# Performance work log

Hardware: AMD Instinct MI355X
Metric: run time of the kernel (lower is better)

Reference implementation:

```python
import jax, jax.numpy as jnp
import numpy as np

NEG_SLOPE = 0.2


def add_self_loops(edge_index, num_nodes):
    loop = jnp.arange(num_nodes, dtype=edge_index.dtype)
    src = jnp.concatenate([edge_index[0], loop])
    dst = jnp.concatenate([edge_index[1], loop])
    return src, dst


def gat_conv(x, src, dst, W, att_src, att_dst, bias, heads, out_ch, concat):
    N = x.shape[0]
    h = (x @ W).reshape(N, heads, out_ch)                      # [N,H,C]
    a_src = jnp.sum(h * att_src, axis=-1)                      # [N,H]
    a_dst = jnp.sum(h * att_dst, axis=-1)                      # [N,H]
    e = a_src[src] + a_dst[dst]                                # [E,H]
    e = jax.nn.leaky_relu(e, NEG_SLOPE)
    # segment softmax over incoming edges of each destination node
    m = jax.ops.segment_max(e, dst, num_segments=N)            # [N,H]
    m = jnp.where(jnp.isfinite(m), m, 0.0)
    ex = jnp.exp(e - m[dst])
    s = jax.ops.segment_sum(ex, dst, num_segments=N)           # [N,H]
    alpha = ex / jnp.where(s[dst] > 0, s[dst], 1.0)            # [E,H]
    msg = alpha[:, :, None] * h[src]                           # [E,H,C]
    out = jax.ops.segment_sum(msg, dst, num_segments=N)        # [N,H,C]
    if concat:
        out = out.reshape(N, heads * out_ch)
    else:
        out = out.mean(axis=1)
    return out + bias


def setup_inputs() -> dict:
    key = jax.random.key(0)
    ks = jax.random.split(key, 10)
    N, F, E, H, C1 = 50000, 128, 800000, 8, 8
    x = jax.random.normal(ks[0], (N, F), dtype=jnp.float32)
    edge_index = jax.random.randint(ks[1], (2, E), 0, N, dtype=jnp.int64)
    sc = 0.1
    W1 = jax.random.normal(ks[2], (F, H * C1), dtype=jnp.float32) * sc
    a_src1 = jax.random.normal(ks[3], (H, C1), dtype=jnp.float32) * sc
    a_dst1 = jax.random.normal(ks[4], (H, C1), dtype=jnp.float32) * sc
    b1 = jnp.zeros((H * C1,), dtype=jnp.float32)
    W2 = jax.random.normal(ks[5], (H * C1, F), dtype=jnp.float32) * sc
    a_src2 = jax.random.normal(ks[6], (1, F), dtype=jnp.float32) * sc
    a_dst2 = jax.random.normal(ks[7], (1, F), dtype=jnp.float32) * sc
    b2 = jnp.zeros((F,), dtype=jnp.float32)
    return {"x": x, "edge_index": edge_index, "W1": W1, "a_src1": a_src1,
            "a_dst1": a_dst1, "b1": b1, "W2": W2, "a_src2": a_src2,
            "a_dst2": a_dst2, "b2": b2}


def reference(x, edge_index, W1, a_src1, a_dst1, b1, W2, a_src2, a_dst2, b2):
    N = x.shape[0]
    src, dst = add_self_loops(edge_index, N)
    h = gat_conv(x, src, dst, W1, a_src1, a_dst1, b1, heads=8, out_ch=8, concat=True)
    h = jax.nn.elu(h)
    out = gat_conv(h, src, dst, W2, a_src2, a_dst2, b2, heads=1, out_ch=x.shape[1], concat=True)
    return out
```

## Files before the change

kernel.cpp:

```cpp
#include <hip/hip_runtime.h>
#include <hip/hip_fp16.h>
#include <math.h>

#define NEG_SLOPE 0.2f

typedef _Float16 f16x8 __attribute__((ext_vector_type(8)));
typedef float    f32x4 __attribute__((ext_vector_type(4)));

__device__ __forceinline__ void get_edge(const int* __restrict__ ei, int E, int e,
                                         int& s, int& d) {
    if (e < E) { s = ei[e]; d = ei[E + e]; }
    else       { s = e - E; d = e - E; }
}

__global__ __launch_bounds__(256) void bucket_count(const int* __restrict__ ei, int E, int ET,
                                                    int* __restrict__ bcnt) {
    __shared__ int lhist[256];
    int t = threadIdx.x;
    lhist[t] = 0;
    __syncthreads();
    int start = blockIdx.x * 4096;
#pragma unroll
    for (int k = 0; k < 16; ++k) {
        int e = start + t + k * 256;
        if (e < ET) { int s, d; get_edge(ei, E, e, s, d); atomicAdd(&lhist[d >> 8], 1); }
    }
    __syncthreads();
    if (lhist[t] > 0) atomicAdd(&bcnt[t], lhist[t]);
}

__global__ void bucket_scan(const int* __restrict__ bcnt, int* __restrict__ bbase,
                            int* __restrict__ bcur, int* __restrict__ row_ptr,
                            int nbuck, int N, int ET) {
    __shared__ int buf[256];
    int t = threadIdx.x;
    int v = (t < nbuck) ? bcnt[t] : 0;
    buf[t] = v;
    __syncthreads();
    for (int off = 1; off < 256; off <<= 1) {
        int u = (t >= off) ? buf[t - off] : 0;
        __syncthreads();
        buf[t] += u;
        __syncthreads();
    }
    if (t < nbuck) { int ex = buf[t] - v; bbase[t] = ex; bcur[t] = ex; }
    if (t == 0) row_ptr[N] = ET;
}

__global__ __launch_bounds__(256) void bucket_scatter(const int* __restrict__ ei, int E, int ET,
                                                      int* __restrict__ bcur,
                                                      unsigned int* __restrict__ bstore,
                                                      int nbuck) {
    __shared__ int lhist[256], lbase[256], lrank[256], gbase[256];
    __shared__ unsigned int sbuf[4096];
    __shared__ int saddr[4096];
    int t = threadIdx.x;
    int start = blockIdx.x * 4096;
    int cnt = ET - start; if (cnt > 4096) cnt = 4096;
    lhist[t] = 0; lrank[t] = 0;
    __syncthreads();
    int mybuck[16]; unsigned int myval[16];
#pragma unroll
    for (int k = 0; k < 16; ++k) {
        int e = start + t + k * 256;
        mybuck[k] = -1;
        if (e < ET) {
            int s, d; get_edge(ei, E, e, s, d);
            mybuck[k] = d >> 8;
            myval[k] = ((unsigned int)d << 16) | (unsigned int)s;
            atomicAdd(&lhist[mybuck[k]], 1);
        }
    }
    __syncthreads();
    int v = lhist[t];
    lbase[t] = v;
    __syncthreads();
    for (int off = 1; off < 256; off <<= 1) {
        int u = (t >= off) ? lbase[t - off] : 0;
        __syncthreads();
        lbase[t] += u;
        __syncthreads();
    }
    int excl = lbase[t] - v;
    if (t < nbuck && v > 0) gbase[t] = atomicAdd(&bcur[t], v);
    __syncthreads();
    lbase[t] = excl;
    __syncthreads();
#pragma unroll
    for (int k = 0; k < 16; ++k) {
        int b = mybuck[k];
        if (b >= 0) {
            int r = atomicAdd(&lrank[b], 1);
            int idx = lbase[b] + r;
            sbuf[idx] = myval[k];
            saddr[idx] = gbase[b] + r;
        }
    }
    __syncthreads();
    for (int j = t; j < cnt; j += 256)
        bstore[saddr[j]] = sbuf[j];
}

__global__ __launch_bounds__(256) void bucket_csr(const unsigned int* __restrict__ bstore,
                                                  const int* __restrict__ bcnt,
                                                  const int* __restrict__ bbase,
                                                  int* __restrict__ row_ptr,
                                                  int* __restrict__ col, int N) {
    __shared__ int lcnt[256], lexcl[256], lrank[256];
    int b = blockIdx.x, t = threadIdx.x;
    int nb = bcnt[b], base = bbase[b];
    lcnt[t] = 0; lrank[t] = 0;
    __syncthreads();
    for (int i = t; i < nb; i += 256)
        atomicAdd(&lcnt[(bstore[base + i] >> 16) & 255], 1);
    __syncthreads();
    int v = lcnt[t];
    lexcl[t] = v;
    __syncthreads();
    for (int off = 1; off < 256; off <<= 1) {
        int u = (t >= off) ? lexcl[t - off] : 0;
        __syncthreads();
        lexcl[t] += u;
        __syncthreads();
    }
    int ex = lexcl[t] - v;
    __syncthreads();
    lexcl[t] = ex;
    __syncthreads();
    int node = (b << 8) + t;
    if (node < N) row_ptr[node] = base + ex;
    for (int i = t; i < nb; i += 256) {
        unsigned int pk = bstore[base + i];
        int d8 = (pk >> 16) & 255;
        int r = atomicAdd(&lrank[d8], 1);
        col[base + lexcl[d8] + r] = (int)(pk & 0xFFFFu);
    }
}

__global__ __launch_bounds__(256) void gemm1_kernel(const float* __restrict__ x,
                                                    const float* __restrict__ W,
                                                    const float* __restrict__ asrc,
                                                    const float* __restrict__ adst,
                                                    _Float16* __restrict__ hout,
                                                    float* __restrict__ av,
                                                    float* __restrict__ bv, int N,
                                                    int gblocks,
                                                    const float* __restrict__ W2,
                                                    const float* __restrict__ as2,
                                                    const float* __restrict__ ad2,
                                                    float* __restrict__ wa,
                                                    float* __restrict__ wb,
                                                    int* __restrict__ bcnt) {
    if (blockIdx.x == (unsigned)gblocks) {
        int k = threadIdx.x;
        bcnt[k] = 0;
        if (k < 64) {
            const float* wr = W2 + k * 128;
            float sa = 0.f, sb = 0.f;
#pragma unroll 8
            for (int c = 0; c < 128; ++c) {
                float w = wr[c];
                sa = fmaf(w, as2[c], sa);
                sb = fmaf(w, ad2[c], sb);
            }
            wa[k] = sa; wb[k] = sb;
        }
        return;
    }
    __shared__ unsigned int sWu[4096];
    for (int p = threadIdx.x; p < 4096; p += 256) {
        int frag = p >> 8;
        int lane = (p >> 2) & 63;
        int j2   = p & 3;
        int chunk = frag >> 2, nt = frag & 3;
        int k = chunk * 32 + ((lane >> 4) << 3) + (j2 << 1);
        int n = nt * 16 + (lane & 15);
        union { _Float16 h[2]; unsigned int u; } pk;
        pk.h[0] = (_Float16)W[k * 64 + n];
        pk.h[1] = (_Float16)W[(k + 1) * 64 + n];
        sWu[p] = pk.u;
    }
    __syncthreads();

    int lane = threadIdx.x & 63;
    int wid  = threadIdx.x >> 6;
    int rbase = blockIdx.x * 64 + wid * 16;
    int l15 = lane & 15, quad = lane >> 4;
    int rA = rbase + l15; if (rA >= N) rA = N - 1;

    const unsigned int* fragbase = &sWu[lane * 4];
    f32x4 z = {0.f, 0.f, 0.f, 0.f};
    f32x4 acc[4] = {z, z, z, z};

#pragma unroll
    for (int chunk = 0; chunk < 4; ++chunk) {
        const float* xp = x + (size_t)rA * 128 + chunk * 32 + quad * 8;
        float4 f0 = *((const float4*)xp);
        float4 f1 = *((const float4*)(xp + 4));
        f16x8 af;
        af[0] = (_Float16)f0.x; af[1] = (_Float16)f0.y;
        af[2] = (_Float16)f0.z; af[3] = (_Float16)f0.w;
        af[4] = (_Float16)f1.x; af[5] = (_Float16)f1.y;
        af[6] = (_Float16)f1.z; af[7] = (_Float16)f1.w;
#pragma unroll
        for (int t = 0; t < 4; ++t) {
            f16x8 bf = *((const f16x8*)(fragbase + (chunk * 4 + t) * 256));
            acc[t] = __builtin_amdgcn_mfma_f32_16x16x32_f16(af, bf, acc[t], 0, 0, 0);
        }
    }

    float asc[4], adc[4];
#pragma unroll
    for (int t = 0; t < 4; ++t) { asc[t] = asrc[t * 16 + l15]; adc[t] = adst[t * 16 + l15]; }
#pragma unroll
    for (int reg = 0; reg < 4; ++reg) {
        int r = rbase + quad * 4 + reg;
        bool ok = (r < N);
#pragma unroll
        for (int t = 0; t < 4; ++t) {
            float v = acc[t][reg];
            if (ok) hout[(size_t)r * 64 + t * 16 + l15] = (_Float16)v;
            float pa = v * asc[t], pb = v * adc[t];
            pa += __shfl_xor(pa, 1); pb += __shfl_xor(pb, 1);
            pa += __shfl_xor(pa, 2); pb += __shfl_xor(pb, 2);
            pa += __shfl_xor(pa, 4); pb += __shfl_xor(pb, 4);
            if (ok && (lane & 7) == 0) {
                int head = t * 2 + (l15 >> 3);
                av[r * 8 + head] = pa;
                bv[r * 8 + head] = pb;
            }
        }
    }
}

__global__ __launch_bounds__(512) void agg1_kernel(const int* __restrict__ rp,
                                                   const int* __restrict__ col,
                                                   const float* __restrict__ av,
                                                   const float* __restrict__ bv,
                                                   const __half* __restrict__ h1,
                                                   const float* __restrict__ b1,
                                                   const float* __restrict__ wa,
                                                   const float* __restrict__ wb,
                                                   _Float16* __restrict__ out1,
                                                   float* __restrict__ av2,
                                                   float* __restrict__ bv2, int N) {
    int node = blockIdx.x * 8 + (threadIdx.x >> 6);
    int lane = threadIdx.x & 63;
    if (node >= N) return;
    int g = lane >> 3, gl = lane & 7;
    int beg = rp[node], end = rp[node + 1];
    int last = end - 1;
    float bd = bv[node * 8 + gl];
    const uint4* hrow = (const uint4*)h1;

    uint4 z4 = {0u, 0u, 0u, 0u};
    int e = beg + g;
    int c0 = col[e      <= last ? e      : last];
    int c1 = col[e + 8  <= last ? e + 8  : last];
    int c2 = col[e + 16 <= last ? e + 16 : last];
    float av0 = 0.f, av1v = 0.f; uint4 h0 = z4, h1v = z4;
    if (e < end)     { av0  = av[c0 * 8 + gl]; h0  = hrow[(size_t)c0 * 8 + gl]; }
    if (e + 8 < end) { av1v = av[c1 * 8 + gl]; h1v = hrow[(size_t)c1 * 8 + gl]; }

    float s = 0.f, a0 = 0.f, a1 = 0.f, a2 = 0.f, a3 = 0.f,
          a4 = 0.f, a5 = 0.f, a6 = 0.f, a7 = 0.f;
    for (; e < end; e += 8) {
        float av2v = 0.f; uint4 h2 = z4;
        if (e + 16 < end) { av2v = av[c2 * 8 + gl]; h2 = hrow[(size_t)c2 * 8 + gl]; }
        int c3 = col[e + 24 <= last ? e + 24 : last];
        float l = av0 + bd;
        l = l > 0.f ? l : NEG_SLOPE * l;
        float w = __expf(l);
        float2 f0 = __half22float2(*(const __half2*)&h0.x);
        float2 f1 = __half22float2(*(const __half2*)&h0.y);
        float2 f2 = __half22float2(*(const __half2*)&h0.z);
        float2 f3 = __half22float2(*(const __half2*)&h0.w);
        s += w;
        a0 = fmaf(w, f0.x, a0); a1 = fmaf(w, f0.y, a1);
        a2 = fmaf(w, f1.x, a2); a3 = fmaf(w, f1.y, a3);
        a4 = fmaf(w, f2.x, a4); a5 = fmaf(w, f2.y, a5);
        a6 = fmaf(w, f3.x, a6); a7 = fmaf(w, f3.y, a7);
        av0 = av1v; h0 = h1v; av1v = av2v; h1v = h2; c2 = c3;
    }
#pragma unroll
    for (int off = 8; off < 64; off <<= 1) {
        s  += __shfl_xor(s, off);
        a0 += __shfl_xor(a0, off); a1 += __shfl_xor(a1, off);
        a2 += __shfl_xor(a2, off); a3 += __shfl_xor(a3, off);
        a4 += __shfl_xor(a4, off); a5 += __shfl_xor(a5, off);
        a6 += __shfl_xor(a6, off); a7 += __shfl_xor(a7, off);
    }
    float inv = 1.0f / s;
    float4 bb0 = ((const float4*)b1)[gl * 2];
    float4 bb1 = ((const float4*)b1)[gl * 2 + 1];
    float v0 = a0 * inv + bb0.x, v1 = a1 * inv + bb0.y;
    float v2 = a2 * inv + bb0.z, v3 = a3 * inv + bb0.w;
    float v4 = a4 * inv + bb1.x, v5 = a5 * inv + bb1.y;
    float v6 = a6 * inv + bb1.z, v7 = a7 * inv + bb1.w;
    v0 = v0 > 0.f ? v0 : expm1f(v0); v1 = v1 > 0.f ? v1 : expm1f(v1);
    v2 = v2 > 0.f ? v2 : expm1f(v2); v3 = v3 > 0.f ? v3 : expm1f(v3);
    v4 = v4 > 0.f ? v4 : expm1f(v4); v5 = v5 > 0.f ? v5 : expm1f(v5);
    v6 = v6 > 0.f ? v6 : expm1f(v6); v7 = v7 > 0.f ? v7 : expm1f(v7);
    float4 wa0 = ((const float4*)wa)[gl * 2], wa1 = ((const float4*)wa)[gl * 2 + 1];
    float4 wb0 = ((const float4*)wb)[gl * 2], wb1 = ((const float4*)wb)[gl * 2 + 1];
    float pa = v0 * wa0.x + v1 * wa0.y + v2 * wa0.z + v3 * wa0.w
             + v4 * wa1.x + v5 * wa1.y + v6 * wa1.z + v7 * wa1.w;
    float pb = v0 * wb0.x + v1 * wb0.y + v2 * wb0.z + v3 * wb0.w
             + v4 * wb1.x + v5 * wb1.y + v6 * wb1.z + v7 * wb1.w;
    pa += __shfl_xor(pa, 1); pb += __shfl_xor(pb, 1);
    pa += __shfl_xor(pa, 2); pb += __shfl_xor(pb, 2);
    pa += __shfl_xor(pa, 4); pb += __shfl_xor(pb, 4);
    if (lane == 0) { av2[node] = pa; bv2[node] = pb; }
    if (g == 0) {
        f16x8 o;
        o[0] = (_Float16)v0; o[1] = (_Float16)v1; o[2] = (_Float16)v2; o[3] = (_Float16)v3;
        o[4] = (_Float16)v4; o[5] = (_Float16)v5; o[6] = (_Float16)v6; o[7] = (_Float16)v7;
        ((f16x8*)out1)[(size_t)node * 8 + gl] = o;
    }
}

__global__ __launch_bounds__(512) void agg2_kernel(const int* __restrict__ rp,
                                                   const int* __restrict__ col,
                                                   const float* __restrict__ av,
                                                   const float* __restrict__ bv,
                                                   const __half* __restrict__ out1,
                                                   float* __restrict__ agg64, int N) {
    int node = blockIdx.x * 8 + (threadIdx.x >> 6);
    int lane = threadIdx.x & 63;
    if (node >= N) return;
    int g = lane >> 3, gl = lane & 7;
    int beg = rp[node], end = rp[node + 1];
    int last = end - 1;
    float bd = bv[node];
    const uint4* hrow = (const uint4*)out1;

    uint4 z4 = {0u, 0u, 0u, 0u};
    int e = beg + g;
    int c0 = col[e      <= last ? e      : last];
    int c1 = col[e + 8  <= last ? e + 8  : last];
    int c2 = col[e + 16 <= last ? e + 16 : last];
    float av0 = 0.f, av1v = 0.f; uint4 h0 = z4, h1v = z4;
    if (e < end)     { av0  = av[c0]; h0  = hrow[(size_t)c0 * 8 + gl]; }
    if (e + 8 < end) { av1v = av[c1]; h1v = hrow[(size_t)c1 * 8 + gl]; }

    float s = 0.f, a0 = 0.f, a1 = 0.f, a2 = 0.f, a3 = 0.f,
          a4 = 0.f, a5 = 0.f, a6 = 0.f, a7 = 0.f;
    for (; e < end; e += 8) {
        float av2v = 0.f; uint4 h2 = z4;
        if (e + 16 < end) { av2v = av[c2]; h2 = hrow[(size_t)c2 * 8 + gl]; }
        int c3 = col[e + 24 <= last ? e + 24 : last];
        float l = av0 + bd;
        l = l > 0.f ? l : NEG_SLOPE * l;
        float w = __expf(l);
        float2 f0 = __half22float2(*(const __half2*)&h0.x);
        float2 f1 = __half22float2(*(const __half2*)&h0.y);
        float2 f2 = __half22float2(*(const __half2*)&h0.z);
        float2 f3 = __half22float2(*(const __half2*)&h0.w);
        s += w;
        a0 = fmaf(w, f0.x, a0); a1 = fmaf(w, f0.y, a1);
        a2 = fmaf(w, f1.x, a2); a3 = fmaf(w, f1.y, a3);
        a4 = fmaf(w, f2.x, a4); a5 = fmaf(w, f2.y, a5);
        a6 = fmaf(w, f3.x, a6); a7 = fmaf(w, f3.y, a7);
        av0 = av1v; h0 = h1v; av1v = av2v; h1v = h2; c2 = c3;
    }
#pragma unroll
    for (int off = 8; off < 64; off <<= 1) {
        s  += __shfl_xor(s, off);
        a0 += __shfl_xor(a0, off); a1 += __shfl_xor(a1, off);
        a2 += __shfl_xor(a2, off); a3 += __shfl_xor(a3, off);
        a4 += __shfl_xor(a4, off); a5 += __shfl_xor(a5, off);
        a6 += __shfl_xor(a6, off); a7 += __shfl_xor(a7, off);
    }
    if (g == 0) {
        float inv = 1.0f / s;
        ((float4*)agg64)[(size_t)node * 16 + gl * 2] =
            make_float4(a0 * inv, a1 * inv, a2 * inv, a3 * inv);
        ((float4*)agg64)[(size_t)node * 16 + gl * 2 + 1] =
            make_float4(a4 * inv, a5 * inv, a6 * inv, a7 * inv);
    }
}

__global__ __launch_bounds__(256) void gemm2_kernel(const float* __restrict__ he,
                                                    const float* __restrict__ W,
                                                    const float* __restrict__ b2,
                                                    float* __restrict__ dout, int N) {
    __shared__ unsigned int sWu[4096];
    for (int p = threadIdx.x; p < 4096; p += 256) {
        int frag = p >> 8;
        int lane = (p >> 2) & 63;
        int j2   = p & 3;
        int chunk = frag >> 3, nt = frag & 7;
        int k = chunk * 32 + ((lane >> 4) << 3) + (j2 << 1);
        int n = nt * 16 + (lane & 15);
        union { _Float16 h[2]; unsigned int u; } pk;
        pk.h[0] = (_Float16)W[k * 128 + n];
        pk.h[1] = (_Float16)W[(k + 1) * 128 + n];
        sWu[p] = pk.u;
    }
    __syncthreads();

    int lane = threadIdx.x & 63;
    int wid  = threadIdx.x >> 6;
    int rbase = blockIdx.x * 64 + wid * 16;
    int l15 = lane & 15, quad = lane >> 4;
    int rA = rbase + l15; if (rA >= N) rA = N - 1;

    const unsigned int* fragbase = &sWu[lane * 4];
    f32x4 z = {0.f, 0.f, 0.f, 0.f};
    f32x4 acc[8] = {z, z, z, z, z, z, z, z};

#pragma unroll
    for (int chunk = 0; chunk < 2; ++chunk) {
        const float* xp = he + (size_t)rA * 64 + chunk * 32 + quad * 8;
        float4 f0 = *((const float4*)xp);
        float4 f1 = *((const float4*)(xp + 4));
        f16x8 af;
        af[0] = (_Float16)f0.x; af[1] = (_Float16)f0.y;
        af[2] = (_Float16)f0.z; af[3] = (_Float16)f0.w;
        af[4] = (_Float16)f1.x; af[5] = (_Float16)f1.y;
        af[6] = (_Float16)f1.z; af[7] = (_Float16)f1.w;
#pragma unroll
        for (int t = 0; t < 8; ++t) {
            f16x8 bf = *((const f16x8*)(fragbase + (chunk * 8 + t) * 256));
            acc[t] = __builtin_amdgcn_mfma_f32_16x16x32_f16(af, bf, acc[t], 0, 0, 0);
        }
    }

    float bcol[8];
#pragma unroll
    for (int t = 0; t < 8; ++t) bcol[t] = b2[t * 16 + l15];
#pragma unroll
    for (int reg = 0; reg < 4; ++reg) {
        int r = rbase + quad * 4 + reg;
        if (r < N) {
#pragma unroll
            for (int t = 0; t < 8; ++t)
                dout[(size_t)r * 128 + t * 16 + l15] = acc[t][reg] + bcol[t];
        }
    }
}

extern "C" void kernel_launch(void* const* d_in, const int* in_sizes, int n_in,
                              void* d_out, int out_size, void* d_ws, size_t ws_size,
                              hipStream_t stream) {
    const float* x      = (const float*)d_in[0];
    const int*   ei     = (const int*)  d_in[1];
    const float* W1     = (const float*)d_in[2];
    const float* a_src1 = (const float*)d_in[3];
    const float* a_dst1 = (const float*)d_in[4];
    const float* b1     = (const float*)d_in[5];
    const float* W2     = (const float*)d_in[6];
    const float* a_src2 = (const float*)d_in[7];
    const float* a_dst2 = (const float*)d_in[8];
    const float* b2     = (const float*)d_in[9];
    float* dout = (float*)d_out;

    const int N  = in_sizes[0] / 128;
    const int E  = in_sizes[1] / 2;
    const int ET = E + N;
    const int NBUCK = (N + 255) >> 8;
    const int NBLKA = (ET + 4095) >> 12;

    char* wsb = (char*)d_ws;
    _Float16* h1   = (_Float16*)wsb; wsb += (size_t)N * 64 * 2;
    _Float16* out1 = (_Float16*)wsb; wsb += (size_t)N * 64 * 2;
    float* agg64 = (float*)wsb; wsb += (size_t)N * 64 * 4;
    float* av1  = (float*)wsb; wsb += (size_t)N * 8 * 4;
    float* bv1  = (float*)wsb; wsb += (size_t)N * 8 * 4;
    float* av2  = (float*)wsb; wsb += (size_t)N * 4;
    float* bv2  = (float*)wsb; wsb += (size_t)N * 4;
    float* wa   = (float*)wsb; wsb += 64 * 4;
    float* wb   = (float*)wsb; wsb += 64 * 4;
    int* row_ptr = (int*)wsb; wsb += (size_t)(N + 1) * 4;
    int* col     = (int*)wsb; wsb += (size_t)ET * 4;
    unsigned int* bstore = (unsigned int*)wsb; wsb += (size_t)ET * 4;
    int* bcnt  = (int*)wsb; wsb += 256 * 4;
    int* bbase = (int*)wsb; wsb += 256 * 4;
    int* bcur  = (int*)wsb; wsb += 256 * 4;

    const int B = 256;
    const int gblocks = (N + 63) / 64;

    gemm1_kernel<<<gblocks + 1, B, 0, stream>>>(x, W1, a_src1, a_dst1, h1, av1, bv1, N,
                                                gblocks, W2, a_src2, a_dst2, wa, wb, bcnt);

    bucket_count<<<NBLKA, B, 0, stream>>>(ei, E, ET, bcnt);
    bucket_scan<<<1, B, 0, stream>>>(bcnt, bbase, bcur, row_ptr, NBUCK, N, ET);
    bucket_scatter<<<NBLKA, B, 0, stream>>>(ei, E, ET, bcur, bstore, NBUCK);
    bucket_csr<<<NBUCK, B, 0, stream>>>(bstore, bcnt, bbase, row_ptr, col, N);

    agg1_kernel<<<(N + 7) / 8, 512, 0, stream>>>(row_ptr, col, av1, bv1, (const __half*)h1,
                                                 b1, wa, wb, out1, av2, bv2, N);

    agg2_kernel<<<(N + 7) / 8, 512, 0, stream>>>(row_ptr, col, av2, bv2,
                                                 (const __half*)out1, agg64, N);
    gemm2_kernel<<<gblocks, B, 0, stream>>>(agg64, W2, b2, dout, N);
}
```

Before: 217.0 us.

## Replace bucket count and scan with fixed-capacity strided buckets

```diff
diff --git a/kernel.cpp b/kernel.cpp
--- a/kernel.cpp
+++ b/kernel.cpp
@@ -3,6 +3,7 @@
 #include <math.h>
 
 #define NEG_SLOPE 0.2f
+#define BSTRIDE 6144
 
 typedef _Float16 f16x8 __attribute__((ext_vector_type(8)));
 typedef float    f32x4 __attribute__((ext_vector_type(4)));
@@ -11,40 +12,6 @@
                                          int& s, int& d) {
     if (e < E) { s = ei[e]; d = ei[E + e]; }
     else       { s = e - E; d = e - E; }
-}
-
-__global__ __launch_bounds__(256) void bucket_count(const int* __restrict__ ei, int E, int ET,
-                                                    int* __restrict__ bcnt) {
-    __shared__ int lhist[256];
-    int t = threadIdx.x;
-    lhist[t] = 0;
-    __syncthreads();
-    int start = blockIdx.x * 4096;
-#pragma unroll
-    for (int k = 0; k < 16; ++k) {
-        int e = start + t + k * 256;
-        if (e < ET) { int s, d; get_edge(ei, E, e, s, d); atomicAdd(&lhist[d >> 8], 1); }
-    }
-    __syncthreads();
-    if (lhist[t] > 0) atomicAdd(&bcnt[t], lhist[t]);
-}
-
-__global__ void bucket_scan(const int* __restrict__ bcnt, int* __restrict__ bbase,
-                            int* __restrict__ bcur, int* __restrict__ row_ptr,
-                            int nbuck, int N, int ET) {
-    __shared__ int buf[256];
-    int t = threadIdx.x;
-    int v = (t < nbuck) ? bcnt[t] : 0;
-    buf[t] = v;
-    __syncthreads();
-    for (int off = 1; off < 256; off <<= 1) {
-        int u = (t >= off) ? buf[t - off] : 0;
-        __syncthreads();
-        buf[t] += u;
-        __syncthreads();
-    }
-    if (t < nbuck) { int ex = buf[t] - v; bbase[t] = ex; bcur[t] = ex; }
-    if (t == 0) row_ptr[N] = ET;
 }
 
 __global__ __launch_bounds__(256) void bucket_scatter(const int* __restrict__ ei, int E, int ET,
@@ -102,13 +69,14 @@
 }
 
 __global__ __launch_bounds__(256) void bucket_csr(const unsigned int* __restrict__ bstore,
-                                                  const int* __restrict__ bcnt,
-                                                  const int* __restrict__ bbase,
-                                                  int* __restrict__ row_ptr,
+                                                  const int* __restrict__ bcur,
+                                                  int* __restrict__ row_beg,
+                                                  int* __restrict__ row_end,
                                                   int* __restrict__ col, int N) {
     __shared__ int lcnt[256], lexcl[256], lrank[256];
     int b = blockIdx.x, t = threadIdx.x;
-    int nb = bcnt[b], base = bbase[b];
+    int base = b * BSTRIDE;
+    int nb = bcur[b] - base;
     lcnt[t] = 0; lrank[t] = 0;
     __syncthreads();
     for (int i = t; i < nb; i += 256)
@@ -128,7 +96,10 @@
     lexcl[t] = ex;
     __syncthreads();
     int node = (b << 8) + t;
-    if (node < N) row_ptr[node] = base + ex;
+    if (node < N) {
+        row_beg[node] = base + ex;
+        row_end[node] = base + ex + v;
+    }
     for (int i = t; i < nb; i += 256) {
         unsigned int pk = bstore[base + i];
         int d8 = (pk >> 16) & 255;
@@ -150,10 +121,10 @@
                                                     const float* __restrict__ ad2,
                                                     float* __restrict__ wa,
                                                     float* __restrict__ wb,
-                                                    int* __restrict__ bcnt) {
+                                                    int* __restrict__ bcur) {
     if (blockIdx.x == (unsigned)gblocks) {
         int k = threadIdx.x;
-        bcnt[k] = 0;
+        bcur[k] = k * BSTRIDE;
         if (k < 64) {
             const float* wr = W2 + k * 128;
             float sa = 0.f, sb = 0.f;
@@ -233,7 +204,8 @@
     }
 }
 
-__global__ __launch_bounds__(512) void agg1_kernel(const int* __restrict__ rp,
+__global__ __launch_bounds__(512) void agg1_kernel(const int* __restrict__ rbeg,
+                                                   const int* __restrict__ rend,
                                                    const int* __restrict__ col,
                                                    const float* __restrict__ av,
                                                    const float* __restrict__ bv,
@@ -248,7 +220,7 @@
     int lane = threadIdx.x & 63;
     if (node >= N) return;
     int g = lane >> 3, gl = lane & 7;
-    int beg = rp[node], end = rp[node + 1];
+    int beg = rbeg[node], end = rend[node];
     int last = end - 1;
     float bd = bv[node * 8 + gl];
     const uint4* hrow = (const uint4*)h1;
@@ -319,7 +291,8 @@
     }
 }
 
-__global__ __launch_bounds__(512) void agg2_kernel(const int* __restrict__ rp,
+__global__ __launch_bounds__(512) void agg2_kernel(const int* __restrict__ rbeg,
+                                                   const int* __restrict__ rend,
                                                    const int* __restrict__ col,
                                                    const float* __restrict__ av,
                                                    const float* __restrict__ bv,
@@ -329,7 +302,7 @@
     int lane = threadIdx.x & 63;
     if (node >= N) return;
     int g = lane >> 3, gl = lane & 7;
-    int beg = rp[node], end = rp[node + 1];
+    int beg = rbeg[node], end = rend[node];
     int last = end - 1;
     float bd = bv[node];
     const uint4* hrow = (const uint4*)out1;
@@ -471,28 +444,26 @@
     float* bv2  = (float*)wsb; wsb += (size_t)N * 4;
     float* wa   = (float*)wsb; wsb += 64 * 4;
     float* wb   = (float*)wsb; wsb += 64 * 4;
-    int* row_ptr = (int*)wsb; wsb += (size_t)(N + 1) * 4;
-    int* col     = (int*)wsb; wsb += (size_t)ET * 4;
-    unsigned int* bstore = (unsigned int*)wsb; wsb += (size_t)ET * 4;
-    int* bcnt  = (int*)wsb; wsb += 256 * 4;
-    int* bbase = (int*)wsb; wsb += 256 * 4;
+    int* row_beg = (int*)wsb; wsb += (size_t)N * 4;
+    int* row_end = (int*)wsb; wsb += (size_t)N * 4;
+    int* col     = (int*)wsb; wsb += (size_t)NBUCK * BSTRIDE * 4;
+    unsigned int* bstore = (unsigned int*)wsb; wsb += (size_t)NBUCK * BSTRIDE * 4;
     int* bcur  = (int*)wsb; wsb += 256 * 4;
 
     const int B = 256;
     const int gblocks = (N + 63) / 64;
 
     gemm1_kernel<<<gblocks + 1, B, 0, stream>>>(x, W1, a_src1, a_dst1, h1, av1, bv1, N,
-                                                gblocks, W2, a_src2, a_dst2, wa, wb, bcnt);
-
-    bucket_count<<<NBLKA, B, 0, stream>>>(ei, E, ET, bcnt);
-    bucket_scan<<<1, B, 0, stream>>>(bcnt, bbase, bcur, row_ptr, NBUCK, N, ET);
+                                                gblocks, W2, a_src2, a_dst2, wa, wb, bcur);
+
     bucket_scatter<<<NBLKA, B, 0, stream>>>(ei, E, ET, bcur, bstore, NBUCK);
-    bucket_csr<<<NBUCK, B, 0, stream>>>(bstore, bcnt, bbase, row_ptr, col, N);
-
-    agg1_kernel<<<(N + 7) / 8, 512, 0, stream>>>(row_ptr, col, av1, bv1, (const __half*)h1,
-                                                 b1, wa, wb, out1, av2, bv2, N);
-
-    agg2_kernel<<<(N + 7) / 8, 512, 0, stream>>>(row_ptr, col, av2, bv2,
+    bucket_csr<<<NBUCK, B, 0, stream>>>(bstore, bcur, row_beg, row_end, col, N);
+
+    agg1_kernel<<<(N + 7) / 8, 512, 0, stream>>>(row_beg, row_end, col, av1, bv1,
+                                                 (const __half*)h1, b1, wa, wb,
+                                                 out1, av2, bv2, N);
+
+    agg2_kernel<<<(N + 7) / 8, 512, 0, stream>>>(row_beg, row_end, col, av2, bv2,
                                                  (const __half*)out1, agg64, N);
     gemm2_kernel<<<gblocks, B, 0, stream>>>(agg64, W2, b2, dout, N);
 }
```

Result: faster. 201.6 us (-7.1%).
